# Optimization experiments

Measured on AMD Instinct MI355X. Metric: run time of the kernel, lower is better.

Reference implementation:

```python
import jax, jax.numpy as jnp
import numpy as np

N, B, E, H, D, L, NT = 30000, 16, 60000, 128, 64, 2, 5


def _build_graph():
    rng = np.random.default_rng(0)
    ng = N // B
    row = rng.integers(0, N, size=E)
    g = row // ng
    col = g * ng + rng.integers(0, ng, size=E)  # bonds stay within a graph
    order = np.argsort(g, kind='stable')        # sort bonds by graph id
    row, col = row[order], col[order]
    edge_index = np.stack([row, col]).astype(np.int32)
    # bond graph: bonds adjacent iff they share an atom (vectorized _build_bond_graph)
    atoms = np.concatenate([row, col])
    bonds = np.concatenate([np.arange(E), np.arange(E)])
    o2 = np.argsort(atoms, kind='stable')
    sb = bonds[o2]
    counts = np.bincount(atoms, minlength=N)
    offs = np.concatenate([[0], np.cumsum(counts)[:-1]])
    sq = counts * counts
    total = int(sq.sum())
    gid = np.repeat(np.arange(N), sq)
    poff = np.concatenate([[0], np.cumsum(sq)[:-1]])
    pos = np.arange(total) - np.repeat(poff, sq)
    c, o = counts[gid], offs[gid]
    ii, jj = pos // c, pos % c
    mask = ii != jj
    bond_edge_index = np.stack([sb[o + ii][mask], sb[o + jj][mask]]).astype(np.int32)
    batch = np.repeat(np.arange(B), ng).astype(np.int32)
    return edge_index, bond_edge_index, batch


def setup_inputs() -> dict:
    edge_index, bond_edge_index, batch = _build_graph()
    key = jax.random.key(0)
    ks = jax.random.split(key, 16)
    s = 0.05
    n = lambda k, shp: jax.random.normal(k, shp, jnp.float32) * s
    return {
        'atom_features': jax.random.normal(ks[0], (N, H), jnp.float32),
        'atom_pos': jax.random.normal(ks[1], (N, 3), jnp.float32),
        'atomic_numbers': jax.random.randint(ks[2], (N,), 1, 20, jnp.int32),
        'batch': jnp.asarray(batch),
        'edge_index': jnp.asarray(edge_index),
        'bond_edge_index': jnp.asarray(bond_edge_index),
        'iw1': n(ks[3], (2 * H, D)), 'ib1': jnp.zeros((D,), jnp.float32),
        'iw2': n(ks[4], (D, D)), 'ib2': jnp.zeros((D,), jnp.float32),
        'emb': n(ks[5], (L, NT, D)),
        'mw1': n(ks[6], (L, 3 * D, D)), 'mb1': jnp.zeros((L, D), jnp.float32),
        'mw2': n(ks[7], (L, D, D)), 'mb2': jnp.zeros((L, D), jnp.float32),
        'uw1': n(ks[8], (L, 2 * D, D)), 'ub1': jnp.zeros((L, D), jnp.float32),
        'uw2': n(ks[9], (L, D, D)), 'ub2': jnp.zeros((L, D), jnp.float32),
        'num_graphs': B,
    }


def reference(atom_features, atom_pos, iw1, ib1, iw2, ib2, emb, mw1, mb1, mw2, mb2,
              uw1, ub1, uw2, ub2, atomic_numbers, batch, edge_index, bond_edge_index,
              num_graphs):
    row, col = edge_index
    hi, hj = atom_features[row], atom_features[col]  # [E, H] gathers
    # bond_init MLP
    x = jax.nn.silu(jnp.concatenate([hi, hj], -1) @ iw1 + ib1) @ iw2 + ib2  # [E, D]
    # _classify_bonds: cosine-similarity thresholds (order matters, matches torch)
    ni = jnp.maximum(jnp.linalg.norm(hi, axis=-1), 1e-8)
    nj = jnp.maximum(jnp.linalg.norm(hj, axis=-1), 1e-8)
    sim = jnp.sum(hi * hj, -1) / (ni * nj)
    bt = jnp.where(sim > 0.8, 1, 0)
    bt = jnp.where(sim > 0.9, 2, bt)
    bt = jnp.where(sim < 0.3, 3, bt)
    src, dst = bond_edge_index  # x_j = x[src], x_i = x[dst]; aggregate at dst
    nb = x.shape[0]
    deg = jax.ops.segment_sum(jnp.ones(src.shape, jnp.float32), dst, num_segments=nb)
    denom = jnp.maximum(deg, 1.0)[:, None]  # PyG mean aggr: 0 for isolated nodes
    for l in range(mw1.shape[0]):
        te = emb[l][bt]  # [E, D] bond-type embedding
        msg_in = jnp.concatenate([x[dst], x[src], te[dst]], -1)  # [BE, 3D]
        msg = jax.nn.silu(msg_in @ mw1[l] + mb1[l]) @ mw2[l] + mb2[l]
        aggr = jax.ops.segment_sum(msg, dst, num_segments=nb) / denom
        upd_in = jnp.concatenate([aggr, x], -1)
        x = x + jax.nn.silu(upd_in @ uw1[l] + ub1[l]) @ uw2[l] + ub2[l]
    # pooling: edges are sorted by graph, so repeat_interleave == batch[row]
    bond_batch = batch[row]
    cnt = jax.ops.segment_sum(jnp.ones((nb,), jnp.float32), bond_batch, num_segments=num_graphs)
    gfeat = jax.ops.segment_sum(x, bond_batch, num_segments=num_graphs) / jnp.maximum(cnt, 1.0)[:, None]
    return x, gfeat
```

## Files before the change

kernel.cpp:

```cpp
#include <hip/hip_runtime.h>
#include <cstdint>
#include <cstddef>

#define HDIM 128
#define DDIM 64
#define NTYPES 5
#define NGRAPHS 16
#define PCHUNK 128
#define EPB 64
#define APW 8

typedef __attribute__((ext_vector_type(8))) short short8;
typedef __attribute__((ext_vector_type(4))) float f32x4;

static __device__ __forceinline__ short8 as_s8(uint4 u) {
    return __builtin_bit_cast(short8, u);
}

static __device__ __forceinline__ float silu_f(float v) {
    return v * __builtin_amdgcn_rcpf(1.0f + __expf(-v));
}

static __device__ __forceinline__ float4 ld4(const float* p) {
    return *reinterpret_cast<const float4*>(p);
}

static __device__ __forceinline__ void st4(float* p, float4 v) {
    *reinterpret_cast<float4*>(p) = v;
}

static __device__ __forceinline__ float4 add4(float4 a, float4 b) {
    return make_float4(a.x + b.x, a.y + b.y, a.z + b.z, a.w + b.w);
}

static __device__ __forceinline__ void silu_acc4(float4& s, float4 v) {
    s.x += silu_f(v.x);
    s.y += silu_f(v.y);
    s.z += silu_f(v.z);
    s.w += silu_f(v.w);
}

static __device__ __forceinline__ unsigned int bf16r(float f) {
    unsigned int u = __float_as_uint(f);
    return (u + 0x7FFFu + ((u >> 16) & 1u)) >> 16;
}
static __device__ __forceinline__ uint4 pack8(const float* f) {
    uint4 r;
    r.x = bf16r(f[0]) | (bf16r(f[1]) << 16);
    r.y = bf16r(f[2]) | (bf16r(f[3]) << 16);
    r.z = bf16r(f[4]) | (bf16r(f[5]) << 16);
    r.w = bf16r(f[6]) | (bf16r(f[7]) << 16);
    return r;
}
static __device__ __forceinline__ void unpack8(uint4 u, float4& a, float4& b) {
    a.x = __uint_as_float(u.x << 16);
    a.y = __uint_as_float(u.x & 0xFFFF0000u);
    a.z = __uint_as_float(u.y << 16);
    a.w = __uint_as_float(u.y & 0xFFFF0000u);
    b.x = __uint_as_float(u.z << 16);
    b.y = __uint_as_float(u.z & 0xFFFF0000u);
    b.z = __uint_as_float(u.w << 16);
    b.w = __uint_as_float(u.w & 0xFFFF0000u);
}

static __device__ __forceinline__ void hilo8(const float* f, uint4& h, uint4& lo) {
    h = pack8(f);
    float4 a, b;
    unpack8(h, a, b);
    float g[8] = {f[0] - a.x, f[1] - a.y, f[2] - a.z, f[3] - a.w,
                  f[4] - b.x, f[5] - b.y, f[6] - b.z, f[7] - b.w};
    lo = pack8(g);
}

static __device__ __forceinline__ int xcd_logical_block() {
    int chunk = (int)(gridDim.x >> 3);
    return (int)(blockIdx.x & 7) * chunk + (int)(blockIdx.x >> 3);
}

__global__ void __launch_bounds__(256) count_k(const int* __restrict__ bdst,
                                               int* __restrict__ cnt, int BE) {
    int i = blockIdx.x * 256 + threadIdx.x;
    if (i < BE)
        __hip_atomic_fetch_add(&cnt[bdst[i]], 1, __ATOMIC_RELAXED, __HIP_MEMORY_SCOPE_AGENT);
}

__global__ void __launch_bounds__(256) bsum_k(const int* __restrict__ cnt,
                                              int* __restrict__ bsum, int E) {
    __shared__ int red[256];
    int t = threadIdx.x;
    int i = blockIdx.x * 256 + t;
    red[t] = (i < E) ? cnt[i] : 0;
    __syncthreads();
    #pragma unroll
    for (int off = 128; off > 0; off >>= 1) {
        if (t < off) red[t] += red[t + off];
        __syncthreads();
    }
    if (t == 0) bsum[blockIdx.x] = red[0];
}

__global__ void __launch_bounds__(1024) bscan_k(const int* __restrict__ bsum,
                                                int* __restrict__ bpre, int NB) {
    __shared__ int sh[1024];
    int t = threadIdx.x;
    int v0 = (t < NB) ? bsum[t] : 0;
    sh[t] = v0;
    __syncthreads();
    for (int off = 1; off < 1024; off <<= 1) {
        int v = (t >= off) ? sh[t - off] : 0;
        __syncthreads();
        sh[t] += v;
        __syncthreads();
    }
    if (t < NB) bpre[t] = sh[t] - v0;
}

__global__ void __launch_bounds__(256) offs_k(const int* __restrict__ cnt,
                                              const int* __restrict__ bpre,
                                              int* __restrict__ offs,
                                              int* __restrict__ cursor, int E) {
    __shared__ int sh[256];
    int t = threadIdx.x;
    int i = blockIdx.x * 256 + t;
    int v0 = (i < E) ? cnt[i] : 0;
    sh[t] = v0;
    __syncthreads();
    for (int off = 1; off < 256; off <<= 1) {
        int v = (t >= off) ? sh[t - off] : 0;
        __syncthreads();
        sh[t] += v;
        __syncthreads();
    }
    int ex = sh[t] - v0 + bpre[blockIdx.x];
    if (i < E) { offs[i] = ex; cursor[i] = ex; }
    if (i == E - 1) offs[E] = ex + v0;
}

__global__ void __launch_bounds__(256) scatter_k(const int* __restrict__ bsrc,
                                                 const int* __restrict__ bdst,
                                                 int* __restrict__ cursor,
                                                 int* __restrict__ srclist, int BE) {
    int i = blockIdx.x * 256 + threadIdx.x;
    if (i < BE) {
        int d = bdst[i];
        int p = __hip_atomic_fetch_add(&cursor[d], 1, __ATOMIC_RELAXED,
                                       __HIP_MEMORY_SCOPE_AGENT);
        srclist[p] = bsrc[i];
    }
}

__global__ void __launch_bounds__(64) tt2_k(const float* __restrict__ emb,
                                            const float* __restrict__ mw1,
                                            const float* __restrict__ mb1,
                                            float* __restrict__ tt) {
    int b = blockIdx.x;
    int l = b / NTYPES, t = b % NTYPES, j = threadIdx.x;
    const float* embl = emb + (size_t)l * NTYPES * DDIM + (size_t)t * DDIM;
    const float* w1 = mw1 + (size_t)l * 192 * DDIM;
    float s = mb1[l * DDIM + j];
    #pragma unroll 8
    for (int k = 0; k < DDIM; ++k)
        s = fmaf(embl[k], w1[(HDIM + k) * DDIM + j], s);
    tt[(size_t)b * DDIM + j] = s;
}

__global__ void __launch_bounds__(64) fuse_k(const float* __restrict__ mw2,
                                             const float* __restrict__ mb2,
                                             const float* __restrict__ uw1,
                                             float* __restrict__ w2u,
                                             float* __restrict__ b2u) {
    int l = blockIdx.x >> 6, k = blockIdx.x & 63, j = threadIdx.x;
    const float* w2 = mw2 + (size_t)l * DDIM * DDIM;
    const float* u1 = uw1 + (size_t)l * 128 * DDIM;
    float s = 0.f;
    #pragma unroll 8
    for (int t = 0; t < DDIM; ++t)
        s = fmaf(w2[k * DDIM + t], u1[(size_t)t * DDIM + j], s);
    w2u[(size_t)l * DDIM * DDIM + (size_t)k * DDIM + j] = s;
    if (k == 0) {
        float b = 0.f;
        #pragma unroll 8
        for (int t = 0; t < DDIM; ++t)
            b = fmaf(mb2[l * DDIM + t], u1[(size_t)t * DDIM + j], b);
        b2u[l * DDIM + j] = b;
    }
}

__global__ void __launch_bounds__(64) packall_k(const float* __restrict__ w2u,
                                                const float* __restrict__ uw1,
                                                const float* __restrict__ uw2,
                                                const float* __restrict__ mw1,
                                                uint4* __restrict__ fw2u,
                                                uint4* __restrict__ fu1b,
                                                uint4* __restrict__ fu2,
                                                uint4* __restrict__ fp) {
    int b = blockIdx.x;
    int mat = b >> 3, jt = (b >> 1) & 3, ks = b & 1, l = threadIdx.x;
    const float* src;
    uint4* dst;
    switch (mat) {
        case 0: src = w2u;                         dst = fw2u;        break;
        case 1: src = w2u + 4096;                  dst = fw2u + 1024; break;
        case 2: src = uw1 + 64 * 64;               dst = fu1b;        break;
        case 3: src = uw1 + 128 * 64 + 64 * 64;    dst = fu1b + 1024; break;
        case 4: src = uw2;                         dst = fu2;         break;
        case 5: src = uw2 + 4096;                  dst = fu2 + 1024;  break;
        case 6: src = mw1 + (size_t)192 * 64;      dst = fp;          break;
        default: src = mw1 + (size_t)192 * 64 + 64 * 64; dst = fp + 1024; break;
    }
    int k0 = ks * 32 + (l >> 4) * 8;
    int j = jt * 16 + (l & 15);
    float f[8];
    #pragma unroll
    for (int i = 0; i < 8; ++i) f[i] = src[(size_t)(k0 + i) * 64 + j];
    uint4 h, lo;
    hilo8(f, h, lo);
    size_t di = ((size_t)(jt * 2 + ks) * 64 + l) * 2;
    dst[di] = h;
    dst[di + 1] = lo;
}

static __device__ __forceinline__ int slotIdx(int row, int slot) {
    return row * 8 + (slot ^ (row & 7));
}

static __device__ __forceinline__ short8 ldFragA(const uint4* buf, int rowBase, int lane, int ks) {
    int row = rowBase + (lane & 15);
    int slot = ks * 4 + (lane >> 4);
    return as_s8(buf[slotIdx(row, slot)]);
}

static __device__ __forceinline__ void loadB(const uint4* __restrict__ frag, int jt, int lane,
                                             short8& h0, short8& h1, short8& l0, short8& l1) {
    const uint4* p0 = frag + ((size_t)(jt * 2 + 0) * 64 + lane) * 2;
    const uint4* p1 = frag + ((size_t)(jt * 2 + 1) * 64 + lane) * 2;
    h0 = as_s8(p0[0]); l0 = as_s8(p0[1]);
    h1 = as_s8(p1[0]); l1 = as_s8(p1[1]);
}

static __device__ __forceinline__ f32x4 gemm_tile(const uint4* Ahi, const uint4* Alo,
        int rowBase, int lane,
        short8 bh0, short8 bh1, short8 bl0, short8 bl1, f32x4 acc) {
    short8 ah0 = ldFragA(Ahi, rowBase, lane, 0);
    short8 ah1 = ldFragA(Ahi, rowBase, lane, 1);
    short8 al0 = ldFragA(Alo, rowBase, lane, 0);
    short8 al1 = ldFragA(Alo, rowBase, lane, 1);
    acc = __builtin_amdgcn_mfma_f32_16x16x32_bf16(ah0, bh0, acc, 0, 0, 0);
    acc = __builtin_amdgcn_mfma_f32_16x16x32_bf16(ah1, bh1, acc, 0, 0, 0);
    acc = __builtin_amdgcn_mfma_f32_16x16x32_bf16(al0, bh0, acc, 0, 0, 0);
    acc = __builtin_amdgcn_mfma_f32_16x16x32_bf16(al1, bh1, acc, 0, 0, 0);
    acc = __builtin_amdgcn_mfma_f32_16x16x32_bf16(ah0, bl0, acc, 0, 0, 0);
    acc = __builtin_amdgcn_mfma_f32_16x16x32_bf16(ah1, bl1, acc, 0, 0, 0);
    return acc;
}

__global__ void __launch_bounds__(256) atom_proj_k(
    const float* __restrict__ AF, const float* __restrict__ iw1,
    float* __restrict__ pa, float* __restrict__ qa, float* __restrict__ na, int N) {
    int lane = threadIdx.x & 63;
    int w = __builtin_amdgcn_readfirstlane((int)(threadIdx.x >> 6));
    int abase = blockIdx.x * (4 * APW) + w * APW;
    if (abase >= N) return;

    float accp[APW], accq[APW], nrm[APW];
    #pragma unroll
    for (int a = 0; a < APW; ++a) { accp[a] = 0.f; accq[a] = 0.f; nrm[a] = 0.f; }

    #pragma unroll 4
    for (int k = 0; k < HDIM; k += 4) {
        float wt[4], wb[4];
        #pragma unroll
        for (int kk = 0; kk < 4; ++kk) {
            wt[kk] = iw1[(size_t)(k + kk) * DDIM + lane];
            wb[kk] = iw1[(size_t)(HDIM + k + kk) * DDIM + lane];
        }
        #pragma unroll
        for (int a = 0; a < APW; ++a) {
            int aa = min(abase + a, N - 1);
            float4 hv = ld4(AF + (size_t)aa * HDIM + k);
            accp[a] = fmaf(hv.x, wt[0], accp[a]);
            accp[a] = fmaf(hv.y, wt[1], accp[a]);
            accp[a] = fmaf(hv.z, wt[2], accp[a]);
            accp[a] = fmaf(hv.w, wt[3], accp[a]);
            accq[a] = fmaf(hv.x, wb[0], accq[a]);
            accq[a] = fmaf(hv.y, wb[1], accq[a]);
            accq[a] = fmaf(hv.z, wb[2], accq[a]);
            accq[a] = fmaf(hv.w, wb[3], accq[a]);
            nrm[a] = fmaf(hv.x, hv.x, nrm[a]);
            nrm[a] = fmaf(hv.y, hv.y, nrm[a]);
            nrm[a] = fmaf(hv.z, hv.z, nrm[a]);
            nrm[a] = fmaf(hv.w, hv.w, nrm[a]);
        }
    }
    #pragma unroll
    for (int a = 0; a < APW; ++a) {
        int atom = abase + a;
        if (atom < N) {
            pa[(size_t)atom * DDIM + lane] = accp[a];
            qa[(size_t)atom * DDIM + lane] = accq[a];
            if (lane == 0) na[atom] = sqrtf(nrm[a]);
        }
    }
}

__global__ void __launch_bounds__(512) bond_init2_k(
    const float* __restrict__ AF, const int* __restrict__ row, const int* __restrict__ col,
    const float* __restrict__ pa, const float* __restrict__ qa, const float* __restrict__ na,
    const float* __restrict__ b1, const float* __restrict__ w2, const float* __restrict__ b2,
    const float* __restrict__ w1p ,
    float* __restrict__ x, int* __restrict__ bt,
    float* __restrict__ pd, uint4* __restrict__ ps, int E) {
    __shared__ float hbuf[EPB][DDIM + 1];
    __shared__ float dotb[EPB][8];
    int nEB = (E + EPB - 1) / EPB;
    int lb = xcd_logical_block();
    if (lb >= nEB) return;
    int tid = threadIdx.x;
    int lane = tid & 63;
    int w = __builtin_amdgcn_readfirstlane((int)(tid >> 6));
    int e = lb * EPB + lane;
    bool ok = e < E;
    int eidx = ok ? e : 0;
    int r = row[eidx], c = col[eidx];
    int j0 = w * 8;

    {
        const float* hi = AF + (size_t)r * HDIM + w * 16;
        const float* hj = AF + (size_t)c * HDIM + w * 16;
        float d = 0.f;
        #pragma unroll
        for (int k = 0; k < 16; k += 4) {
            float4 a4 = ld4(hi + k), b4 = ld4(hj + k);
            d += a4.x * b4.x + a4.y * b4.y + a4.z * b4.z + a4.w * b4.w;
        }
        dotb[lane][w] = d;
    }

    {
        const float* pr = pa + (size_t)r * DDIM + j0;
        const float* qc = qa + (size_t)c * DDIM + j0;
        float4 p0 = ld4(pr + 0), p1 = ld4(pr + 4);
        float4 q0 = ld4(qc + 0), q1 = ld4(qc + 4);
        hbuf[lane][j0 + 0] = silu_f(p0.x + q0.x + b1[j0 + 0]);
        hbuf[lane][j0 + 1] = silu_f(p0.y + q0.y + b1[j0 + 1]);
        hbuf[lane][j0 + 2] = silu_f(p0.z + q0.z + b1[j0 + 2]);
        hbuf[lane][j0 + 3] = silu_f(p0.w + q0.w + b1[j0 + 3]);
        hbuf[lane][j0 + 4] = silu_f(p1.x + q1.x + b1[j0 + 4]);
        hbuf[lane][j0 + 5] = silu_f(p1.y + q1.y + b1[j0 + 5]);
        hbuf[lane][j0 + 6] = silu_f(p1.z + q1.z + b1[j0 + 6]);
        hbuf[lane][j0 + 7] = silu_f(p1.w + q1.w + b1[j0 + 7]);
    }
    __syncthreads();

    if (w == 0) {
        float dot = dotb[lane][0] + dotb[lane][1] + dotb[lane][2] + dotb[lane][3]
                  + dotb[lane][4] + dotb[lane][5] + dotb[lane][6] + dotb[lane][7];
        float nr = fmaxf(na[r], 1e-8f), nc = fmaxf(na[c], 1e-8f);
        float sim = dot / (nr * nc);
        int t = 0;
        if (sim > 0.8f) t = 1;
        if (sim > 0.9f) t = 2;
        if (sim < 0.3f) t = 3;
        if (ok) bt[e] = t;
    }

    float o[8];
    #pragma unroll
    for (int jj = 0; jj < 8; ++jj) o[jj] = b2[j0 + jj];
    #pragma unroll 4
    for (int k = 0; k < DDIM; ++k) {
        float hk = hbuf[lane][k];
        const float* wk = w2 + (size_t)k * DDIM + j0;
        #pragma unroll
        for (int jj = 0; jj < 8; ++jj) o[jj] = fmaf(hk, wk[jj], o[jj]);
    }
    if (ok) {
        float* xr = x + (size_t)e * DDIM + j0;
        st4(xr + 0, make_float4(o[0], o[1], o[2], o[3]));
        st4(xr + 4, make_float4(o[4], o[5], o[6], o[7]));
    }
    __syncthreads();
    #pragma unroll
    for (int jj = 0; jj < 8; ++jj) hbuf[lane][j0 + jj] = o[jj];
    __syncthreads();

    float apd[8], aps[8];
    #pragma unroll
    for (int jj = 0; jj < 8; ++jj) { apd[jj] = 0.f; aps[jj] = 0.f; }
    #pragma unroll 4
    for (int k = 0; k < DDIM; ++k) {
        float xk = hbuf[lane][k];
        const float* wd = w1p + (size_t)k * DDIM + j0;
        const float* wsv = w1p + (size_t)(DDIM + k) * DDIM + j0;
        #pragma unroll
        for (int jj = 0; jj < 8; ++jj) {
            apd[jj] = fmaf(xk, wd[jj], apd[jj]);
            aps[jj] = fmaf(xk, wsv[jj], aps[jj]);
        }
    }
    if (ok) {
        float* pr = pd + (size_t)e * DDIM + j0;
        st4(pr + 0, make_float4(apd[0], apd[1], apd[2], apd[3]));
        st4(pr + 4, make_float4(apd[4], apd[5], apd[6], apd[7]));
        ps[(size_t)e * 8 + w] = pack8(aps);
    }
}

__global__ void __launch_bounds__(256) proj_k(const float* __restrict__ x,
                                              const float* __restrict__ w1 ,
                                              float* __restrict__ pd, uint4* __restrict__ ps,
                                              int E) {
    int lane = threadIdx.x & 63;
    int w = __builtin_amdgcn_readfirstlane((int)(threadIdx.x >> 6));
    int e = blockIdx.x * EPB + lane;
    bool ok = e < E;
    int eidx = ok ? e : 0;
    int j0 = w * 16;
    const float* xr = x + (size_t)eidx * DDIM;

    float apd[16], aps[16];
    #pragma unroll
    for (int jj = 0; jj < 16; ++jj) { apd[jj] = 0.f; aps[jj] = 0.f; }
    #pragma unroll 2
    for (int c = 0; c < 16; ++c) {
        float4 v = ld4(xr + c * 4);
        float xv[4] = {v.x, v.y, v.z, v.w};
        #pragma unroll
        for (int kk = 0; kk < 4; ++kk) {
            int k = c * 4 + kk;
            const float* wd = w1 + (size_t)k * DDIM + j0;
            const float* wsv = w1 + (size_t)(DDIM + k) * DDIM + j0;
            #pragma unroll
            for (int jj = 0; jj < 16; ++jj) {
                apd[jj] = fmaf(xv[kk], wd[jj], apd[jj]);
                aps[jj] = fmaf(xv[kk], wsv[jj], aps[jj]);
            }
        }
    }
    if (ok) {
        float* pr = pd + (size_t)e * DDIM + j0;
        st4(pr + 0,  make_float4(apd[0],  apd[1],  apd[2],  apd[3]));
        st4(pr + 4,  make_float4(apd[4],  apd[5],  apd[6],  apd[7]));
        st4(pr + 8,  make_float4(apd[8],  apd[9],  apd[10], apd[11]));
        st4(pr + 12, make_float4(apd[12], apd[13], apd[14], apd[15]));
        ps[(size_t)e * 8 + 2 * w + 0] = pack8(aps + 0);
        ps[(size_t)e * 8 + 2 * w + 1] = pack8(aps + 8);
    }
}

__global__ void __launch_bounds__(512, 4) layer_k(
    float* __restrict__ x, const float* __restrict__ pd, const uint4* __restrict__ ps,
    const float* __restrict__ tt_l, const int* __restrict__ bt,
    const int* __restrict__ offs, const int* __restrict__ srclist,
    const int* __restrict__ cnt,
    const uint4* __restrict__ fW2u, const float* __restrict__ b2u,
    const uint4* __restrict__ fU1b, const float* __restrict__ ub1,
    const uint4* __restrict__ fU2, const float* __restrict__ ub2,
    const uint4* __restrict__ fP ,
    float* __restrict__ pdn, uint4* __restrict__ psn, int E) {
    __shared__ uint4 sAhi[512];
    __shared__ uint4 sAlo[512];
    __shared__ uint4 sXhi[512];
    __shared__ uint4 sXlo[512];
    __shared__ float degLDS[64];
    int nEB = (E + EPB - 1) / EPB;
    int lb = xcd_logical_block();
    if (lb >= nEB) return;
    int tid = threadIdx.x;
    int lane = tid & 63;
    int w = __builtin_amdgcn_readfirstlane((int)(tid >> 6));
    int e0 = lb * EPB;

    {
        int dl = tid >> 3, q = tid & 7;
        int d = e0 + dl;
        bool ok = d < E;
        int dd = ok ? d : 0;
        int jq = q * 8;
        const float* xr = x + (size_t)dd * DDIM + jq;
        float4 xv0 = ld4(xr + 0), xv1 = ld4(xr + 4);
        int dc = cnt[dd];
        const float* pr = pd + (size_t)dd * DDIM + jq;
        const float* tp = tt_l + (size_t)bt[dd] * DDIM + jq;
        float4 b0 = add4(ld4(pr + 0), ld4(tp + 0));
        float4 b1 = add4(ld4(pr + 4), ld4(tp + 4));
        float4 s0 = make_float4(0, 0, 0, 0), s1 = s0;
        int p0 = ok ? offs[d] : 0, p1 = ok ? offs[d + 1] : 0;
        int p = p0;
        for (; p + 4 <= p1; p += 4) {
            uint4 u0 = ps[(size_t)srclist[p + 0] * 8 + q];
            uint4 u1 = ps[(size_t)srclist[p + 1] * 8 + q];
            uint4 u2 = ps[(size_t)srclist[p + 2] * 8 + q];
            uint4 u3 = ps[(size_t)srclist[p + 3] * 8 + q];
            float4 a, b;
            unpack8(u0, a, b);
            silu_acc4(s0, add4(b0, a));
            silu_acc4(s1, add4(b1, b));
            unpack8(u1, a, b);
            silu_acc4(s0, add4(b0, a));
            silu_acc4(s1, add4(b1, b));
            unpack8(u2, a, b);
            silu_acc4(s0, add4(b0, a));
            silu_acc4(s1, add4(b1, b));
            unpack8(u3, a, b);
            silu_acc4(s0, add4(b0, a));
            silu_acc4(s1, add4(b1, b));
        }
        for (; p < p1; ++p) {
            uint4 u0 = ps[(size_t)srclist[p] * 8 + q];
            float4 a, b;
            unpack8(u0, a, b);
            silu_acc4(s0, add4(b0, a));
            silu_acc4(s1, add4(b1, b));
        }
        float inv = 1.0f / fmaxf((float)dc, 1.0f);
        float sv[8] = {s0.x * inv, s0.y * inv, s0.z * inv, s0.w * inv,
                       s1.x * inv, s1.y * inv, s1.z * inv, s1.w * inv};
        float xf[8] = {xv0.x, xv0.y, xv0.z, xv0.w, xv1.x, xv1.y, xv1.z, xv1.w};
        if (!ok) {
            #pragma unroll
            for (int i = 0; i < 8; ++i) { sv[i] = 0.f; xf[i] = 0.f; }
        }
        uint4 h4, l4;
        int si = slotIdx(dl, q);
        hilo8(sv, h4, l4);
        sAhi[si] = h4; sAlo[si] = l4;
        hilo8(xf, h4, l4);
        sXhi[si] = h4; sXlo[si] = l4;
        if (q == 0) degLDS[dl] = (ok && dc > 0) ? 1.0f : 0.0f;
    }
    int jt = w & 3, mh = w >> 2;
    short8 A2h0, A2h1, A2l0, A2l1;
    short8 U1h0, U1h1, U1l0, U1l1;
    loadB(fW2u, jt, lane, A2h0, A2h1, A2l0, A2l1);
    loadB(fU1b, jt, lane, U1h0, U1h1, U1l0, U1l1);
    __syncthreads();

    int rb0 = mh * 32, rb1 = mh * 32 + 16;
    f32x4 z4 = {0.f, 0.f, 0.f, 0.f};
    f32x4 acc0 = z4, acc1 = z4;
    acc0 = gemm_tile(sAhi, sAlo, rb0, lane, A2h0, A2h1, A2l0, A2l1, acc0);
    acc0 = gemm_tile(sXhi, sXlo, rb0, lane, U1h0, U1h1, U1l0, U1l1, acc0);
    acc1 = gemm_tile(sAhi, sAlo, rb1, lane, A2h0, A2h1, A2l0, A2l1, acc1);
    acc1 = gemm_tile(sXhi, sXlo, rb1, lane, U1h0, U1h1, U1l0, U1l1, acc1);
    __syncthreads();
    int j = jt * 16 + (lane & 15);
    float ub1j = ub1[j], b2uj = b2u[j];
    unsigned short* hA = (unsigned short*)sAhi;
    unsigned short* lA = (unsigned short*)sAlo;
    #pragma unroll
    for (int r = 0; r < 4; ++r) {
        int row = rb0 + (lane >> 4) * 4 + r;
        float hv = silu_f(acc0[r] + ub1j + degLDS[row] * b2uj);
        unsigned int hb = bf16r(hv);
        float lov = hv - __uint_as_float(hb << 16);
        int ui = (row * 8 + ((j >> 3) ^ (row & 7))) * 8 + (j & 7);
        hA[ui] = (unsigned short)hb;
        lA[ui] = (unsigned short)bf16r(lov);
    }
    #pragma unroll
    for (int r = 0; r < 4; ++r) {
        int row = rb1 + (lane >> 4) * 4 + r;
        float hv = silu_f(acc1[r] + ub1j + degLDS[row] * b2uj);
        unsigned int hb = bf16r(hv);
        float lov = hv - __uint_as_float(hb << 16);
        int ui = (row * 8 + ((j >> 3) ^ (row & 7))) * 8 + (j & 7);
        hA[ui] = (unsigned short)hb;
        lA[ui] = (unsigned short)bf16r(lov);
    }
    __syncthreads();

    short8 U2h0, U2h1, U2l0, U2l1;
    loadB(fU2, jt, lane, U2h0, U2h1, U2l0, U2l1);
    f32x4 o0 = z4, o1 = z4;
    o0 = gemm_tile(sAhi, sAlo, rb0, lane, U2h0, U2h1, U2l0, U2l1, o0);
    o1 = gemm_tile(sAhi, sAlo, rb1, lane, U2h0, U2h1, U2l0, U2l1, o1);
    float ub2j = ub2[j];
    bool haveP = (fP != nullptr);
    unsigned short* hX = (unsigned short*)sXhi;
    unsigned short* lX = (unsigned short*)sXlo;
    #pragma unroll
    for (int r = 0; r < 4; ++r) {
        int row = rb0 + (lane >> 4) * 4 + r;
        int e = e0 + row;
        float xvv = (e < E) ? x[(size_t)e * DDIM + j] : 0.f;
        float xn = xvv + o0[r] + ub2j;
        if (e < E) x[(size_t)e * DDIM + j] = xn;
        if (haveP) {
            unsigned int hb = bf16r(xn);
            float lov = xn - __uint_as_float(hb << 16);
            int ui = (row * 8 + ((j >> 3) ^ (row & 7))) * 8 + (j & 7);
            hX[ui] = (unsigned short)hb;
            lX[ui] = (unsigned short)bf16r(lov);
        }
    }
    #pragma unroll
    for (int r = 0; r < 4; ++r) {
        int row = rb1 + (lane >> 4) * 4 + r;
        int e = e0 + row;
        float xvv = (e < E) ? x[(size_t)e * DDIM + j] : 0.f;
        float xn = xvv + o1[r] + ub2j;
        if (e < E) x[(size_t)e * DDIM + j] = xn;
        if (haveP) {
            unsigned int hb = bf16r(xn);
            float lov = xn - __uint_as_float(hb << 16);
            int ui = (row * 8 + ((j >> 3) ^ (row & 7))) * 8 + (j & 7);
            hX[ui] = (unsigned short)hb;
            lX[ui] = (unsigned short)bf16r(lov);
        }
    }
    if (!haveP) return;
    __syncthreads();

    const uint4* fPw = (w < 4) ? fP : (fP + 1024);
    int jp = w & 3;
    short8 Ph0, Ph1, Pl0, Pl1;
    loadB(fPw, jp, lane, Ph0, Ph1, Pl0, Pl1);
    f32x4 q0 = z4, q1 = z4, q2 = z4, q3 = z4;
    q0 = gemm_tile(sXhi, sXlo, 0,  lane, Ph0, Ph1, Pl0, Pl1, q0);
    q1 = gemm_tile(sXhi, sXlo, 16, lane, Ph0, Ph1, Pl0, Pl1, q1);
    q2 = gemm_tile(sXhi, sXlo, 32, lane, Ph0, Ph1, Pl0, Pl1, q2);
    q3 = gemm_tile(sXhi, sXlo, 48, lane, Ph0, Ph1, Pl0, Pl1, q3);
    if (w < 4) {
        int jd = jp * 16 + (lane & 15);
        #pragma unroll
        for (int mt = 0; mt < 4; ++mt) {
            f32x4 qq = (mt == 0) ? q0 : (mt == 1) ? q1 : (mt == 2) ? q2 : q3;
            #pragma unroll
            for (int r = 0; r < 4; ++r) {
                int row = mt * 16 + (lane >> 4) * 4 + r;
                int e = e0 + row;
                if (e < E) pdn[(size_t)e * DDIM + jd] = qq[r];
            }
        }
    } else {
        int js = jp * 16 + (lane & 15);
        #pragma unroll
        for (int mt = 0; mt < 4; ++mt) {
            f32x4 qq = (mt == 0) ? q0 : (mt == 1) ? q1 : (mt == 2) ? q2 : q3;
            #pragma unroll
            for (int r = 0; r < 4; ++r) {
                int row = mt * 16 + (lane >> 4) * 4 + r;
                int ui = (row * 8 + ((js >> 3) ^ (row & 7))) * 8 + (js & 7);
                hA[ui] = (unsigned short)bf16r(qq[r]);
            }
        }
    }
    __syncthreads();
    {
        int dl = tid >> 3, q = tid & 7;
        int d = e0 + dl;
        if (d < E) psn[(size_t)d * 8 + q] = sAhi[slotIdx(dl, q)];
    }
}

__global__ void __launch_bounds__(256) pool_k(
    const float* __restrict__ x, const int* __restrict__ row,
    const int* __restrict__ batch, float* __restrict__ gfeat, int E) {
    int lane = threadIdx.x & 63;
    int esub = threadIdx.x >> 6;
    int e0 = blockIdx.x * PCHUNK;
    int e1 = min(e0 + PCHUNK, E);
    float sum = 0.f;
    int cur = -1;
    for (int e = e0 + esub; e < e1; e += 4) {
        int g = batch[row[e]];
        if (g != cur) {
            if (cur >= 0)
                __hip_atomic_fetch_add(&gfeat[cur * DDIM + lane], sum,
                                       __ATOMIC_RELAXED, __HIP_MEMORY_SCOPE_AGENT);
            cur = g;
            sum = 0.f;
        }
        sum += x[(size_t)e * DDIM + lane];
    }
    if (cur >= 0)
        __hip_atomic_fetch_add(&gfeat[cur * DDIM + lane], sum,
                               __ATOMIC_RELAXED, __HIP_MEMORY_SCOPE_AGENT);
}

static __device__ __forceinline__ int lower_bound_bb(const int* __restrict__ row,
                                                     const int* __restrict__ batch,
                                                     int E, int g) {
    int lo = 0, hi = E;
    while (lo < hi) {
        int m = (lo + hi) >> 1;
        if (batch[row[m]] < g) lo = m + 1; else hi = m;
    }
    return lo;
}

__global__ void __launch_bounds__(64) pool_final_k(
    const int* __restrict__ row, const int* __restrict__ batch,
    float* __restrict__ gfeat, int E) {
    int g = blockIdx.x, j = threadIdx.x;
    int s = lower_bound_bb(row, batch, E, g);
    int t = lower_bound_bb(row, batch, E, g + 1);
    float cnt = fmaxf((float)(t - s), 1.0f);
    gfeat[g * DDIM + j] /= cnt;
}

extern "C" void kernel_launch(void* const* d_in, const int* in_sizes, int n_in,
                              void* d_out, int out_size, void* d_ws, size_t ws_size,
                              hipStream_t stream) {
    (void)n_in; (void)out_size;
    const float* AF    = (const float*)d_in[0];
    const int*   batch = (const int*)d_in[3];
    const int*   edge_index      = (const int*)d_in[4];
    const int*   bond_edge_index = (const int*)d_in[5];
    const float* iw1 = (const float*)d_in[6];
    const float* ib1 = (const float*)d_in[7];
    const float* iw2 = (const float*)d_in[8];
    const float* ib2 = (const float*)d_in[9];
    const float* emb = (const float*)d_in[10];
    const float* mw1 = (const float*)d_in[11];
    const float* mb1 = (const float*)d_in[12];
    const float* mw2 = (const float*)d_in[13];
    const float* mb2 = (const float*)d_in[14];
    const float* uw1 = (const float*)d_in[15];
    const float* ub1 = (const float*)d_in[16];
    const float* uw2 = (const float*)d_in[17];
    const float* ub2 = (const float*)d_in[18];

    const int N  = in_sizes[0] / HDIM;
    const int E  = in_sizes[4] / 2;
    const int BE = in_sizes[5] / 2;
    const int NB = (E + 255) / 256;
    const int EB = (E + EPB - 1) / EPB;
    const int AB = (N + 4 * APW - 1) / (4 * APW);
    const int EBS = ((EB + 7) / 8) * 8;
    const int PB = (E + PCHUNK - 1) / PCHUNK;

    float* xout  = (float*)d_out;
    float* gfeat = xout + (size_t)E * DDIM;

    char* w = (char*)d_ws;
    float* tt       = (float*)w;  w += sizeof(float) * 2 * NTYPES * DDIM;
    float* w2u      = (float*)w;  w += sizeof(float) * 2 * DDIM * DDIM;
    float* b2u      = (float*)w;  w += sizeof(float) * 2 * DDIM;
    w = (char*)(((uintptr_t)w + 15) & ~(uintptr_t)15);
    uint4* fW2u     = (uint4*)w;  w += 2048 * sizeof(uint4);
    uint4* fU1b     = (uint4*)w;  w += 2048 * sizeof(uint4);
    uint4* fU2      = (uint4*)w;  w += 2048 * sizeof(uint4);
    uint4* fP       = (uint4*)w;  w += 2048 * sizeof(uint4);
    int*   cnt      = (int*)w;    w += sizeof(int) * E;
    int*   offs     = (int*)w;    w += sizeof(int) * (E + 1);
    int*   cursor   = (int*)w;    w += sizeof(int) * E;
    int*   bt       = (int*)w;    w += sizeof(int) * E;
    int*   bsum     = (int*)w;    w += sizeof(int) * 1024;
    int*   bpre     = (int*)w;    w += sizeof(int) * 1024;
    int*   srclist  = (int*)w;    w += sizeof(int) * BE;
    w = (char*)(((uintptr_t)w + 15) & ~(uintptr_t)15);
    float* pd       = (float*)w;  w += sizeof(float) * (size_t)E * DDIM;
    uint4* ps       = (uint4*)w;  w += sizeof(unsigned short) * (size_t)E * DDIM;
    float* pa       = (float*)w;  w += sizeof(float) * (size_t)N * DDIM;
    float* qa       = (float*)w;  w += sizeof(float) * (size_t)N * DDIM;
    float* na       = (float*)w;  w += sizeof(float) * (size_t)N;
    w = (char*)(((uintptr_t)w + 15) & ~(uintptr_t)15);
    float* pd2      = (float*)w;  w += sizeof(float) * (size_t)E * DDIM;
    uint4* ps2      = (uint4*)w;  w += sizeof(unsigned short) * (size_t)E * DDIM;
    bool fuse_proj = ((size_t)(w - (char*)d_ws) <= ws_size);

    const int* row  = edge_index;
    const int* col  = edge_index + E;
    const int* bsrc = bond_edge_index;
    const int* bdst = bond_edge_index + BE;

    hipMemsetAsync(cnt, 0, (size_t)E * sizeof(int), stream);
    count_k<<<(BE + 255) / 256, 256, 0, stream>>>(bdst, cnt, BE);
    bsum_k<<<NB, 256, 0, stream>>>(cnt, bsum, E);
    bscan_k<<<1, 1024, 0, stream>>>(bsum, bpre, NB);
    offs_k<<<NB, 256, 0, stream>>>(cnt, bpre, offs, cursor, E);
    scatter_k<<<(BE + 255) / 256, 256, 0, stream>>>(bsrc, bdst, cursor, srclist, BE);

    tt2_k<<<2 * NTYPES, 64, 0, stream>>>(emb, mw1, mb1, tt);
    fuse_k<<<2 * 64, 64, 0, stream>>>(mw2, mb2, uw1, w2u, b2u);
    packall_k<<<64, 64, 0, stream>>>(w2u, uw1, uw2, mw1, fW2u, fU1b, fU2, fP);

    atom_proj_k<<<AB, 256, 0, stream>>>(AF, iw1, pa, qa, na, N);
    bond_init2_k<<<EBS, 512, 0, stream>>>(AF, row, col, pa, qa, na, ib1, iw2, ib2,
                                          mw1 , xout, bt, pd, ps, E);

    if (fuse_proj) {
        layer_k<<<EBS, 512, 0, stream>>>(
            xout, pd, ps, tt, bt, offs, srclist, cnt,
            fW2u, b2u, fU1b, ub1, fU2, ub2,
            fP, pd2, ps2, E);
        layer_k<<<EBS, 512, 0, stream>>>(
            xout, pd2, ps2, tt + NTYPES * DDIM, bt, offs, srclist, cnt,
            fW2u + 1024, b2u + DDIM, fU1b + 1024, ub1 + DDIM,
            fU2 + 1024, ub2 + DDIM,
            nullptr, nullptr, nullptr, E);
    } else {
        for (int l = 0; l < 2; ++l) {
            if (l > 0)
                proj_k<<<EB, 256, 0, stream>>>(xout, mw1 + (size_t)l * 192 * 64, pd, ps, E);
            layer_k<<<EBS, 512, 0, stream>>>(
                xout, pd, ps, tt + (size_t)l * NTYPES * DDIM, bt, offs, srclist, cnt,
                fW2u + (size_t)l * 1024, b2u + (size_t)l * DDIM,
                fU1b + (size_t)l * 1024, ub1 + (size_t)l * DDIM,
                fU2 + (size_t)l * 1024, ub2 + (size_t)l * DDIM,
                nullptr, nullptr, nullptr, E);
        }
    }

    hipMemsetAsync(gfeat, 0, NGRAPHS * DDIM * sizeof(float), stream);
    pool_k<<<PB, 256, 0, stream>>>(xout, row, batch, gfeat, E);
    pool_final_k<<<NGRAPHS, 64, 0, stream>>>(row, batch, gfeat, E);
}
```

Baseline: 339.1 us.

## Move bond init MLP and first projection onto split-bf16 MFMA tiles

The bond initialisation kernel now computes the second init layer (iw2) and the layer-0 message projections using MFMA gemm tiles over hi/lo bf16 split operands in swizzled shared memory, replacing the scalar FP32 FMA loops. The weights are pre-packed by extending packall_k with three extra matrices. The cosine-similarity dot product is reduced with wave shuffles instead of a shared-memory buffer, and launch bounds now request higher occupancy. The aim is to cut the ALU cost of per-edge 64x64 matmuls, at the price of split-precision numerics and more shared-memory traffic.

```diff
diff --git a/kernel.cpp b/kernel.cpp
--- a/kernel.cpp
+++ b/kernel.cpp
@@ -190,10 +190,13 @@
                                                 const float* __restrict__ uw1,
                                                 const float* __restrict__ uw2,
                                                 const float* __restrict__ mw1,
+                                                const float* __restrict__ iw2,
                                                 uint4* __restrict__ fw2u,
                                                 uint4* __restrict__ fu1b,
                                                 uint4* __restrict__ fu2,
-                                                uint4* __restrict__ fp) {
+                                                uint4* __restrict__ fp,
+                                                uint4* __restrict__ fiw2,
+                                                uint4* __restrict__ fp0) {
     int b = blockIdx.x;
     int mat = b >> 3, jt = (b >> 1) & 3, ks = b & 1, l = threadIdx.x;
     const float* src;
@@ -206,7 +209,10 @@
         case 4: src = uw2;                         dst = fu2;         break;
         case 5: src = uw2 + 4096;                  dst = fu2 + 1024;  break;
         case 6: src = mw1 + (size_t)192 * 64;      dst = fp;          break;
-        default: src = mw1 + (size_t)192 * 64 + 64 * 64; dst = fp + 1024; break;
+        case 7: src = mw1 + (size_t)192 * 64 + 64 * 64; dst = fp + 1024; break;
+        case 8: src = iw2;                         dst = fiw2;        break;
+        case 9: src = mw1;                         dst = fp0;         break;
+        default: src = mw1 + (size_t)64 * 64;      dst = fp0 + 1024;  break;
     }
     int k0 = ks * 32 + (l >> 4) * 8;
     int j = jt * 16 + (l & 15);
@@ -303,106 +309,156 @@
     }
 }
 
-__global__ void __launch_bounds__(512) bond_init2_k(
+__global__ void __launch_bounds__(512, 4) bond_init2_k(
     const float* __restrict__ AF, const int* __restrict__ row, const int* __restrict__ col,
     const float* __restrict__ pa, const float* __restrict__ qa, const float* __restrict__ na,
-    const float* __restrict__ b1, const float* __restrict__ w2, const float* __restrict__ b2,
-    const float* __restrict__ w1p ,
+    const float* __restrict__ b1, const uint4* __restrict__ fW2, const float* __restrict__ b2,
+    const uint4* __restrict__ fP0,
     float* __restrict__ x, int* __restrict__ bt,
     float* __restrict__ pd, uint4* __restrict__ ps, int E) {
-    __shared__ float hbuf[EPB][DDIM + 1];
-    __shared__ float dotb[EPB][8];
+    __shared__ uint4 sAhi[512];
+    __shared__ uint4 sAlo[512];
+    __shared__ uint4 sXhi[512];
+    __shared__ uint4 sXlo[512];
     int nEB = (E + EPB - 1) / EPB;
     int lb = xcd_logical_block();
     if (lb >= nEB) return;
     int tid = threadIdx.x;
     int lane = tid & 63;
     int w = __builtin_amdgcn_readfirstlane((int)(tid >> 6));
-    int e = lb * EPB + lane;
-    bool ok = e < E;
-    int eidx = ok ? e : 0;
-    int r = row[eidx], c = col[eidx];
-    int j0 = w * 8;
+    int e0 = lb * EPB;
 
     {
-        const float* hi = AF + (size_t)r * HDIM + w * 16;
-        const float* hj = AF + (size_t)c * HDIM + w * 16;
-        float d = 0.f;
+        int dl = tid >> 3, q = tid & 7;
+        int d = e0 + dl;
+        bool ok = d < E;
+        int dd = ok ? d : 0;
+        int r = row[dd], c = col[dd];
+        int jq = q * 8;
+
+        const float* hi = AF + (size_t)r * HDIM + q * 16;
+        const float* hj = AF + (size_t)c * HDIM + q * 16;
+        float dt = 0.f;
         #pragma unroll
         for (int k = 0; k < 16; k += 4) {
             float4 a4 = ld4(hi + k), b4 = ld4(hj + k);
-            d += a4.x * b4.x + a4.y * b4.y + a4.z * b4.z + a4.w * b4.w;
-        }
-        dotb[lane][w] = d;
-    }
-
-    {
-        const float* pr = pa + (size_t)r * DDIM + j0;
-        const float* qc = qa + (size_t)c * DDIM + j0;
+            dt += a4.x * b4.x + a4.y * b4.y + a4.z * b4.z + a4.w * b4.w;
+        }
+        dt += __shfl_xor(dt, 1, 64);
+        dt += __shfl_xor(dt, 2, 64);
+        dt += __shfl_xor(dt, 4, 64);
+        if (q == 0 && ok) {
+            float nr = fmaxf(na[r], 1e-8f), nc = fmaxf(na[c], 1e-8f);
+            float sim = dt / (nr * nc);
+            int t = 0;
+            if (sim > 0.8f) t = 1;
+            if (sim > 0.9f) t = 2;
+            if (sim < 0.3f) t = 3;
+            bt[d] = t;
+        }
+
+        const float* pr = pa + (size_t)r * DDIM + jq;
+        const float* qc = qa + (size_t)c * DDIM + jq;
         float4 p0 = ld4(pr + 0), p1 = ld4(pr + 4);
         float4 q0 = ld4(qc + 0), q1 = ld4(qc + 4);
-        hbuf[lane][j0 + 0] = silu_f(p0.x + q0.x + b1[j0 + 0]);
-        hbuf[lane][j0 + 1] = silu_f(p0.y + q0.y + b1[j0 + 1]);
-        hbuf[lane][j0 + 2] = silu_f(p0.z + q0.z + b1[j0 + 2]);
-        hbuf[lane][j0 + 3] = silu_f(p0.w + q0.w + b1[j0 + 3]);
-        hbuf[lane][j0 + 4] = silu_f(p1.x + q1.x + b1[j0 + 4]);
-        hbuf[lane][j0 + 5] = silu_f(p1.y + q1.y + b1[j0 + 5]);
-        hbuf[lane][j0 + 6] = silu_f(p1.z + q1.z + b1[j0 + 6]);
-        hbuf[lane][j0 + 7] = silu_f(p1.w + q1.w + b1[j0 + 7]);
-    }
-    __syncthreads();
-
-    if (w == 0) {
-        float dot = dotb[lane][0] + dotb[lane][1] + dotb[lane][2] + dotb[lane][3]
-                  + dotb[lane][4] + dotb[lane][5] + dotb[lane][6] + dotb[lane][7];
-        float nr = fmaxf(na[r], 1e-8f), nc = fmaxf(na[c], 1e-8f);
-        float sim = dot / (nr * nc);
-        int t = 0;
-        if (sim > 0.8f) t = 1;
-        if (sim > 0.9f) t = 2;
-        if (sim < 0.3f) t = 3;
-        if (ok) bt[e] = t;
-    }
-
-    float o[8];
-    #pragma unroll
-    for (int jj = 0; jj < 8; ++jj) o[jj] = b2[j0 + jj];
-    #pragma unroll 4
-    for (int k = 0; k < DDIM; ++k) {
-        float hk = hbuf[lane][k];
-        const float* wk = w2 + (size_t)k * DDIM + j0;
+        float hv[8];
+        hv[0] = silu_f(p0.x + q0.x + b1[jq + 0]);
+        hv[1] = silu_f(p0.y + q0.y + b1[jq + 1]);
+        hv[2] = silu_f(p0.z + q0.z + b1[jq + 2]);
+        hv[3] = silu_f(p0.w + q0.w + b1[jq + 3]);
+        hv[4] = silu_f(p1.x + q1.x + b1[jq + 4]);
+        hv[5] = silu_f(p1.y + q1.y + b1[jq + 5]);
+        hv[6] = silu_f(p1.z + q1.z + b1[jq + 6]);
+        hv[7] = silu_f(p1.w + q1.w + b1[jq + 7]);
+        if (!ok) {
+            #pragma unroll
+            for (int i = 0; i < 8; ++i) hv[i] = 0.f;
+        }
+        uint4 h4, l4;
+        hilo8(hv, h4, l4);
+        int si = slotIdx(dl, q);
+        sAhi[si] = h4; sAlo[si] = l4;
+    }
+    int jt = w & 3, mh = w >> 2;
+    short8 W2h0, W2h1, W2l0, W2l1;
+    loadB(fW2, jt, lane, W2h0, W2h1, W2l0, W2l1);
+    __syncthreads();
+
+    int rb0 = mh * 32, rb1 = mh * 32 + 16;
+    f32x4 z4 = {0.f, 0.f, 0.f, 0.f};
+    f32x4 acc0 = z4, acc1 = z4;
+    acc0 = gemm_tile(sAhi, sAlo, rb0, lane, W2h0, W2h1, W2l0, W2l1, acc0);
+    acc1 = gemm_tile(sAhi, sAlo, rb1, lane, W2h0, W2h1, W2l0, W2l1, acc1);
+    int j = jt * 16 + (lane & 15);
+    float b2j = b2[j];
+    unsigned short* hX = (unsigned short*)sXhi;
+    unsigned short* lX = (unsigned short*)sXlo;
+    #pragma unroll
+    for (int r = 0; r < 4; ++r) {
+        int rowi = rb0 + (lane >> 4) * 4 + r;
+        int e = e0 + rowi;
+        float xn = acc0[r] + b2j;
+        if (e < E) x[(size_t)e * DDIM + j] = xn;
+        unsigned int hb = bf16r(xn);
+        float lov = xn - __uint_as_float(hb << 16);
+        int ui = (rowi * 8 + ((j >> 3) ^ (rowi & 7))) * 8 + (j & 7);
+        hX[ui] = (unsigned short)hb;
+        lX[ui] = (unsigned short)bf16r(lov);
+    }
+    #pragma unroll
+    for (int r = 0; r < 4; ++r) {
+        int rowi = rb1 + (lane >> 4) * 4 + r;
+        int e = e0 + rowi;
+        float xn = acc1[r] + b2j;
+        if (e < E) x[(size_t)e * DDIM + j] = xn;
+        unsigned int hb = bf16r(xn);
+        float lov = xn - __uint_as_float(hb << 16);
+        int ui = (rowi * 8 + ((j >> 3) ^ (rowi & 7))) * 8 + (j & 7);
+        hX[ui] = (unsigned short)hb;
+        lX[ui] = (unsigned short)bf16r(lov);
+    }
+    __syncthreads();
+
+    const uint4* fPw = (w < 4) ? fP0 : (fP0 + 1024);
+    int jp = w & 3;
+    short8 Ph0, Ph1, Pl0, Pl1;
+    loadB(fPw, jp, lane, Ph0, Ph1, Pl0, Pl1);
+    f32x4 q0 = z4, q1 = z4, q2 = z4, q3 = z4;
+    q0 = gemm_tile(sXhi, sXlo, 0,  lane, Ph0, Ph1, Pl0, Pl1, q0);
+    q1 = gemm_tile(sXhi, sXlo, 16, lane, Ph0, Ph1, Pl0, Pl1, q1);
+    q2 = gemm_tile(sXhi, sXlo, 32, lane, Ph0, Ph1, Pl0, Pl1, q2);
+    q3 = gemm_tile(sXhi, sXlo, 48, lane, Ph0, Ph1, Pl0, Pl1, q3);
+    unsigned short* hA = (unsigned short*)sAhi;
+    if (w < 4) {
+        int jd = jp * 16 + (lane & 15);
         #pragma unroll
-        for (int jj = 0; jj < 8; ++jj) o[jj] = fmaf(hk, wk[jj], o[jj]);
-    }
-    if (ok) {
-        float* xr = x + (size_t)e * DDIM + j0;
-        st4(xr + 0, make_float4(o[0], o[1], o[2], o[3]));
-        st4(xr + 4, make_float4(o[4], o[5], o[6], o[7]));
-    }
-    __syncthreads();
-    #pragma unroll
-    for (int jj = 0; jj < 8; ++jj) hbuf[lane][j0 + jj] = o[jj];
-    __syncthreads();
-
-    float apd[8], aps[8];
-    #pragma unroll
-    for (int jj = 0; jj < 8; ++jj) { apd[jj] = 0.f; aps[jj] = 0.f; }
-    #pragma unroll 4
-    for (int k = 0; k < DDIM; ++k) {
-        float xk = hbuf[lane][k];
-        const float* wd = w1p + (size_t)k * DDIM + j0;
-        const float* wsv = w1p + (size_t)(DDIM + k) * DDIM + j0;
+        for (int mt = 0; mt < 4; ++mt) {
+            f32x4 qq = (mt == 0) ? q0 : (mt == 1) ? q1 : (mt == 2) ? q2 : q3;
+            #pragma unroll
+            for (int r = 0; r < 4; ++r) {
+                int rowi = mt * 16 + (lane >> 4) * 4 + r;
+                int e = e0 + rowi;
+                if (e < E) pd[(size_t)e * DDIM + jd] = qq[r];
+            }
+        }
+    } else {
+        int js = jp * 16 + (lane & 15);
         #pragma unroll
-        for (int jj = 0; jj < 8; ++jj) {
-            apd[jj] = fmaf(xk, wd[jj], apd[jj]);
-            aps[jj] = fmaf(xk, wsv[jj], aps[jj]);
-        }
-    }
-    if (ok) {
-        float* pr = pd + (size_t)e * DDIM + j0;
-        st4(pr + 0, make_float4(apd[0], apd[1], apd[2], apd[3]));
-        st4(pr + 4, make_float4(apd[4], apd[5], apd[6], apd[7]));
-        ps[(size_t)e * 8 + w] = pack8(aps);
+        for (int mt = 0; mt < 4; ++mt) {
+            f32x4 qq = (mt == 0) ? q0 : (mt == 1) ? q1 : (mt == 2) ? q2 : q3;
+            #pragma unroll
+            for (int r = 0; r < 4; ++r) {
+                int rowi = mt * 16 + (lane >> 4) * 4 + r;
+                int ui = (rowi * 8 + ((js >> 3) ^ (rowi & 7))) * 8 + (js & 7);
+                hA[ui] = (unsigned short)bf16r(qq[r]);
+            }
+        }
+    }
+    __syncthreads();
+    {
+        int dl = tid >> 3, q = tid & 7;
+        int d = e0 + dl;
+        if (d < E) ps[(size_t)d * 8 + q] = sAhi[slotIdx(dl, q)];
     }
 }
 
@@ -743,6 +799,8 @@
     uint4* fU1b     = (uint4*)w;  w += 2048 * sizeof(uint4);
     uint4* fU2      = (uint4*)w;  w += 2048 * sizeof(uint4);
     uint4* fP       = (uint4*)w;  w += 2048 * sizeof(uint4);
+    uint4* fIw2     = (uint4*)w;  w += 1024 * sizeof(uint4);
+    uint4* fP0      = (uint4*)w;  w += 2048 * sizeof(uint4);
     int*   cnt      = (int*)w;    w += sizeof(int) * E;
     int*   offs     = (int*)w;    w += sizeof(int) * (E + 1);
     int*   cursor   = (int*)w;    w += sizeof(int) * E;
@@ -775,11 +833,12 @@
 
     tt2_k<<<2 * NTYPES, 64, 0, stream>>>(emb, mw1, mb1, tt);
     fuse_k<<<2 * 64, 64, 0, stream>>>(mw2, mb2, uw1, w2u, b2u);
-    packall_k<<<64, 64, 0, stream>>>(w2u, uw1, uw2, mw1, fW2u, fU1b, fU2, fP);
+    packall_k<<<88, 64, 0, stream>>>(w2u, uw1, uw2, mw1, iw2,
+                                     fW2u, fU1b, fU2, fP, fIw2, fP0);
 
     atom_proj_k<<<AB, 256, 0, stream>>>(AF, iw1, pa, qa, na, N);
-    bond_init2_k<<<EBS, 512, 0, stream>>>(AF, row, col, pa, qa, na, ib1, iw2, ib2,
-                                          mw1 , xout, bt, pd, ps, E);
+    bond_init2_k<<<EBS, 512, 0, stream>>>(AF, row, col, pa, qa, na, ib1, fIw2, ib2,
+                                          fP0, xout, bt, pd, ps, E);
 
     if (fuse_proj) {
         layer_k<<<EBS, 512, 0, stream>>>(
```

Result: faster. 319.6 us (-5.7%).
